# Kernel optimization log

Hardware: AMD Instinct MI355X
Metric: run time of the kernel (lower is better)

## Reference

```python
import jax, jax.numpy as jnp
import numpy as np

NUM_LAYERS = 2
HIDDEN = 512


def setup_inputs() -> dict:
    key = jax.random.key(0)
    ks = jax.random.split(key, 5)
    B, T, D, L, H = 32, 512, 512, NUM_LAYERS, HIDDEN
    s = 1.0 / np.sqrt(H)
    return {
        "x": jax.random.normal(ks[0], (B, T, D), dtype=jnp.float32),
        "h0": jnp.zeros((B, L, H), dtype=jnp.float32),
        "c0": jnp.zeros((B, L, H), dtype=jnp.float32),
        "Wx": jax.random.normal(ks[1], (L, 4 * H, D), dtype=jnp.float32) * s,
        "bx": jax.random.normal(ks[2], (L, 4 * H), dtype=jnp.float32) * s,
        "Wh": jax.random.normal(ks[3], (L, 4 * H, H), dtype=jnp.float32) * s,
        "bh": jax.random.normal(ks[4], (L, 4 * H), dtype=jnp.float32) * s,
    }


def _lstm_forward(x, h0, c0, Wx, bx, Wh, bh):
    # x: [B,T,D]; h0,c0: [B,L,H]; Wx/Wh: [L,4H,*]; gate order (i,f,g,o)
    L, H = Wx.shape[0], Wx.shape[2]

    def step(carry, x_t):
        h, c = carry  # [B,L,H]
        inp = x_t  # [B,D]
        new_h, new_c = [], []
        for l in range(L):
            gates = (inp @ Wx[l].T + bx[l]) + (h[:, l] @ Wh[l].T + bh[l])  # [B,4H]
            i_g, f_g, g_g, o_g = jnp.split(gates, 4, axis=-1)
            c_l = jax.nn.sigmoid(f_g) * c[:, l] + jax.nn.sigmoid(i_g) * jnp.tanh(g_g)
            h_l = jax.nn.sigmoid(o_g) * jnp.tanh(c_l)
            new_h.append(h_l)
            new_c.append(c_l)
            inp = h_l
        return (jnp.stack(new_h, axis=1), jnp.stack(new_c, axis=1)), inp

    (h_n, c_n), ys = jax.lax.scan(step, (h0, c0), jnp.swapaxes(x, 0, 1))
    output = jnp.swapaxes(ys, 0, 1)  # [B,T,H]
    # torch module returns h_n/c_n swapped to [num_layers, batch, hidden]
    return output, (jnp.swapaxes(h_n, 0, 1), jnp.swapaxes(c_n, 0, 1))


def reference(x, h0, c0, Wx, bx, Wh, bh):
    return _lstm_forward(x, h0, c0, Wx, bx, Wh, bh)
```

## Files before the change

### kernel.cpp

```cpp
#include <hip/hip_runtime.h>
#include <hip/hip_bf16.h>

typedef __bf16 bf16x8 __attribute__((ext_vector_type(8)));
typedef float f32x4 __attribute__((ext_vector_type(4)));
typedef unsigned long long u64;

#define MFMA16(a, b, c) __builtin_amdgcn_mfma_f32_16x16x32_bf16((a), (b), (c), 0, 0, 0)

#define HN_OFF 8388608ull
#define CN_OFF 8421376ull

__device__ __forceinline__ float sigf(float x) { return 1.0f / (1.0f + __expf(-x)); }
__device__ __forceinline__ float b2f(unsigned short u) {
    union { unsigned u; float f; } c; c.u = ((unsigned)u) << 16; return c.f;
}
__device__ __forceinline__ unsigned short f2u(float f) {
    __hip_bfloat16 h = __float2bfloat16(f); return *(unsigned short*)&h;
}

__device__ __forceinline__ u64 gload8(const void* p) {
    return __hip_atomic_load((const u64*)p, __ATOMIC_RELAXED, __HIP_MEMORY_SCOPE_AGENT);
}
__device__ __forceinline__ void gstore4(void* p, unsigned v) {
    __hip_atomic_store((unsigned*)p, v, __ATOMIC_RELAXED, __HIP_MEMORY_SCOPE_AGENT);
}

__device__ __forceinline__ void split8(const float* p, bf16x8& hi, bf16x8& lo) {
    union { __hip_bfloat16 h[8]; bf16x8 v; } uh, ul;
    #pragma unroll
    for (int i = 0; i < 8; ++i) {
        __hip_bfloat16 e = __float2bfloat16(p[i]);
        uh.h[i] = e;
        ul.h[i] = __float2bfloat16(p[i] - __bfloat162float(e));
    }
    hi = uh.v; lo = ul.v;
}

__global__ __launch_bounds__(256) void lstm_detect(
    const unsigned* __restrict__ Wq, unsigned* __restrict__ dflag,
    unsigned* __restrict__ flags)
{
    for (int j = threadIdx.x; j < 1024; j += 256) flags[j] = 0;
    if (threadIdx.x < 64) {
        int lane = threadIdx.x;
        int bad = 0;
        #pragma unroll
        for (int i = 0; i < 4; ++i) {
            unsigned u = Wq[(size_t)(lane + i * 64) * 4093];
            float v = b2f((unsigned short)(u & 0xFFFFu));
            if (!(v == v) || fabsf(v) > 100.0f) ++bad;
        }
        #pragma unroll
        for (int off = 32; off; off >>= 1) bad += __shfl_down(bad, off, 64);
        if (lane == 0) *dflag = (bad > 32) ? 1u : 0u;
    }
}

__global__ __launch_bounds__(256) void lstm_init(
    const void* __restrict__ h0v, const void* __restrict__ c0v,
    __hip_bfloat16* __restrict__ h0hi, __hip_bfloat16* __restrict__ h0lo,
    __hip_bfloat16* __restrict__ h1hi, __hip_bfloat16* __restrict__ h1lo,
    float* __restrict__ cws, const unsigned* __restrict__ dflag)
{
    const bool f32 = (*dflag != 0);
    int i = blockIdx.x * 256 + threadIdx.x;
    int b = i >> 9, n = i & 511;
    float f0, f1, g0, g1;
    if (f32) {
        const float* h = (const float*)h0v; const float* c = (const float*)c0v;
        f0 = h[(b * 2 + 0) * 512 + n];  f1 = h[(b * 2 + 1) * 512 + n];
        g0 = c[(b * 2 + 0) * 512 + n];  g1 = c[(b * 2 + 1) * 512 + n];
    } else {
        const unsigned short* h = (const unsigned short*)h0v;
        const unsigned short* c = (const unsigned short*)c0v;
        f0 = b2f(h[(b * 2 + 0) * 512 + n]);  f1 = b2f(h[(b * 2 + 1) * 512 + n]);
        g0 = b2f(c[(b * 2 + 0) * 512 + n]);  g1 = b2f(c[(b * 2 + 1) * 512 + n]);
    }
    __hip_bfloat16 e0 = __float2bfloat16(f0), e1 = __float2bfloat16(f1);
    h0hi[i] = e0; h0lo[i] = __float2bfloat16(f0 - __bfloat162float(e0));
    h1hi[i] = e1; h1lo[i] = __float2bfloat16(f1 - __bfloat162float(e1));
    cws[i] = g0;  cws[16384 + i] = g1;
}

__global__ __launch_bounds__(256, 1) void lstm_seq(
    const void* __restrict__ xv,
    const void* __restrict__ Wxv, const void* __restrict__ bxv,
    const void* __restrict__ Whv, const void* __restrict__ bhv,
    __hip_bfloat16* __restrict__ h0hi, __hip_bfloat16* __restrict__ h0lo,
    __hip_bfloat16* __restrict__ h1hi, __hip_bfloat16* __restrict__ h1lo,
    const float* __restrict__ cws, unsigned* __restrict__ flags,
    const unsigned* __restrict__ dflag, void* __restrict__ outv)
{
    const bool f32 = (*dflag != 0);
    const int p  = blockIdx.x & 1;
    const int wt = blockIdx.x >> 1;
    const int tid = threadIdx.x;
    const int q = tid >> 6, lane = tid & 63;
    const int n16 = lane & 15, quad = lane >> 4;
    const int colg = q * 512 + wt * 16 + n16;

    __shared__ __align__(16) char smem[131072];
    __shared__ float gbuf[2176];

    float* outf = (float*)outv;
    __hip_bfloat16* outh = (__hip_bfloat16*)outv;

    bf16x8 wa[16], wal[16], wr[16], wrl[16];
    if (f32) {
        const float* WA = (const float*)Wxv + ((size_t)(p * 2048 + colg)) * 512;
        const float* WR = (const float*)Whv + ((size_t)(p * 2048 + colg)) * 512;
        #pragma unroll
        for (int kk = 0; kk < 16; ++kk) {
            split8(WA + kk * 32 + quad * 8, wa[kk], wal[kk]);
            split8(WR + kk * 32 + quad * 8, wr[kk], wrl[kk]);
        }
    } else {
        const unsigned short* WA = (const unsigned short*)Wxv + ((size_t)(p * 2048 + colg)) * 512;
        const unsigned short* WR = (const unsigned short*)Whv + ((size_t)(p * 2048 + colg)) * 512;
        union { uint4 u; bf16x8 v; } cvu;
        #pragma unroll
        for (int kk = 0; kk < 16; ++kk) {
            cvu.u = *(const uint4*)(WA + kk * 32 + quad * 8); wa[kk] = cvu.v;
            cvu.u = *(const uint4*)(WR + kk * 32 + quad * 8); wr[kk] = cvu.v;
        }
    }
    float bias;
    if (f32) bias = ((const float*)bxv)[p * 2048 + colg] + ((const float*)bhv)[p * 2048 + colg];
    else     bias = b2f(((const unsigned short*)bxv)[p * 2048 + colg])
                  + b2f(((const unsigned short*)bhv)[p * 2048 + colg]);

    const int e0 = tid * 2;
    const int pbb = e0 >> 4;
    const int pn0 = e0 & 15;
    float cv[2];
    cv[0] = cws[p * 16384 + pbb * 512 + wt * 16 + pn0];
    cv[1] = cws[p * 16384 + pbb * 512 + wt * 16 + pn0 + 1];

    const unsigned short* xb = (const unsigned short*)xv;

    #define STAGE_X_BF16(T)                                                      \
        { _Pragma("unroll")                                                      \
          for (int j = 0; j < 8; ++j) {                                          \
              int L = j * 256 + tid;                                             \
              int rem = L & 127;                                                 \
              int row = ((rem >> 6) << 4) + (rem & 15);                          \
              int kcol = ((L >> 7) << 5) + (((rem >> 4) & 3) << 3);              \
              *(uint4*)(smem + (L << 4)) =                                       \
                  *(const uint4*)(xb + ((size_t)row * 512 + (T)) * 512 + kcol);  \
          } }

    if (p == 0 && !f32) STAGE_X_BF16(0);

    for (int k = 0; k <= 512; ++k) {
        const bool doComp = (p == 0) ? (k < 512) : (k > 0);

        if (doComp) {
            const int t = (p == 0) ? k : (k - 1);
            const __hip_bfloat16* Ahi = h0hi + (k & 1) * 16384;
            const __hip_bfloat16* Alo = h0lo + (k & 1) * 16384;
            const __hip_bfloat16* Rhi = (p == 0) ? h0hi + (k & 1) * 16384
                                                 : h1hi + ((k + 1) & 1) * 16384;
            const __hip_bfloat16* Rlo = (p == 0) ? h0lo + (k & 1) * 16384
                                                 : h1lo + ((k + 1) & 1) * 16384;

            if (p == 1) {
                #pragma unroll
                for (int hp = 0; hp < 2; ++hp) {
                    u64 vA[8], vB[8], vR[8], vL[8];
                    #pragma unroll
                    for (int jj = 0; jj < 4; ++jj) {
                        int L = (hp * 4 + jj) * 256 + tid;
                        int rem = L & 127;
                        int row = ((rem >> 6) << 4) + (rem & 15);
                        int kcol = ((L >> 7) << 5) + (((rem >> 4) & 3) << 3);
                        size_t hoff = (size_t)row * 512 + kcol;
                        vA[jj*2] = gload8(Ahi + hoff); vA[jj*2+1] = gload8(Ahi + hoff + 4);
                        vB[jj*2] = gload8(Alo + hoff); vB[jj*2+1] = gload8(Alo + hoff + 4);
                        vR[jj*2] = gload8(Rhi + hoff); vR[jj*2+1] = gload8(Rhi + hoff + 4);
                        vL[jj*2] = gload8(Rlo + hoff); vL[jj*2+1] = gload8(Rlo + hoff + 4);
                    }
                    #pragma unroll
                    for (int jj = 0; jj < 4; ++jj) {
                        int L = (hp * 4 + jj) * 256 + tid;
                        u64* dA = (u64*)(smem + (L << 4));
                        u64* dB = (u64*)(smem + 32768 + (L << 4));
                        u64* dR = (u64*)(smem + 65536 + (L << 4));
                        u64* dL = (u64*)(smem + 98304 + (L << 4));
                        dA[0] = vA[jj*2]; dA[1] = vA[jj*2+1];
                        dB[0] = vB[jj*2]; dB[1] = vB[jj*2+1];
                        dR[0] = vR[jj*2]; dR[1] = vR[jj*2+1];
                        dL[0] = vL[jj*2]; dL[1] = vL[jj*2+1];
                    }
                }
            } else {
                u64 vR[16], vL[16];
                #pragma unroll
                for (int j = 0; j < 8; ++j) {
                    int L = j * 256 + tid;
                    int rem = L & 127;
                    int row = ((rem >> 6) << 4) + (rem & 15);
                    int kcol = ((L >> 7) << 5) + (((rem >> 4) & 3) << 3);
                    size_t hoff = (size_t)row * 512 + kcol;
                    vR[j*2] = gload8(Rhi + hoff); vR[j*2+1] = gload8(Rhi + hoff + 4);
                    vL[j*2] = gload8(Rlo + hoff); vL[j*2+1] = gload8(Rlo + hoff + 4);
                }
                #pragma unroll
                for (int j = 0; j < 8; ++j) {
                    int L = j * 256 + tid;
                    u64* dR = (u64*)(smem + 65536 + (L << 4));
                    u64* dL = (u64*)(smem + 98304 + (L << 4));
                    dR[0] = vR[j*2]; dR[1] = vR[j*2+1];
                    dL[0] = vL[j*2]; dL[1] = vL[j*2+1];
                }
                if (f32) {
                    #pragma unroll
                    for (int j = 0; j < 8; ++j) {
                        int L = j * 256 + tid;
                        int rem = L & 127;
                        int row = ((rem >> 6) << 4) + (rem & 15);
                        int kcol = ((L >> 7) << 5) + (((rem >> 4) & 3) << 3);
                        const float* xp = (const float*)xv + ((size_t)row * 512 + t) * 512 + kcol;
                        bf16x8 hi, lo;
                        split8(xp, hi, lo);
                        *(bf16x8*)(smem + (L << 4)) = hi;
                        *(bf16x8*)(smem + 32768 + (L << 4)) = lo;
                    }
                }
            }
            __syncthreads();

            const char* sl = smem + (lane << 4);
            f32x4 acc0 = {bias, bias, bias, bias};
            f32x4 acc1 = {bias, bias, bias, bias};
            if (f32) {
                #pragma unroll
                for (int kk = 0; kk < 16; ++kk) {
                    bf16x8 Aha = *(const bf16x8*)(sl + kk * 2048);
                    bf16x8 Ahb = *(const bf16x8*)(sl + kk * 2048 + 1024);
                    bf16x8 Ala = *(const bf16x8*)(sl + 32768 + kk * 2048);
                    bf16x8 Alb = *(const bf16x8*)(sl + 32768 + kk * 2048 + 1024);
                    bf16x8 Rha = *(const bf16x8*)(sl + 65536 + kk * 2048);
                    bf16x8 Rhb = *(const bf16x8*)(sl + 65536 + kk * 2048 + 1024);
                    bf16x8 Rla = *(const bf16x8*)(sl + 98304 + kk * 2048);
                    bf16x8 Rlb = *(const bf16x8*)(sl + 98304 + kk * 2048 + 1024);
                    acc0 = MFMA16(Aha, wa[kk], acc0);
                    acc0 = MFMA16(Aha, wal[kk], acc0);
                    acc0 = MFMA16(Ala, wa[kk], acc0);
                    acc0 = MFMA16(Rha, wr[kk], acc0);
                    acc0 = MFMA16(Rha, wrl[kk], acc0);
                    acc0 = MFMA16(Rla, wr[kk], acc0);
                    acc1 = MFMA16(Ahb, wa[kk], acc1);
                    acc1 = MFMA16(Ahb, wal[kk], acc1);
                    acc1 = MFMA16(Alb, wa[kk], acc1);
                    acc1 = MFMA16(Rhb, wr[kk], acc1);
                    acc1 = MFMA16(Rhb, wrl[kk], acc1);
                    acc1 = MFMA16(Rlb, wr[kk], acc1);
                }
            } else if (p == 1) {
                #pragma unroll
                for (int kk = 0; kk < 16; ++kk) {
                    bf16x8 Aha = *(const bf16x8*)(sl + kk * 2048);
                    bf16x8 Ahb = *(const bf16x8*)(sl + kk * 2048 + 1024);
                    bf16x8 Ala = *(const bf16x8*)(sl + 32768 + kk * 2048);
                    bf16x8 Alb = *(const bf16x8*)(sl + 32768 + kk * 2048 + 1024);
                    bf16x8 Rha = *(const bf16x8*)(sl + 65536 + kk * 2048);
                    bf16x8 Rhb = *(const bf16x8*)(sl + 65536 + kk * 2048 + 1024);
                    bf16x8 Rla = *(const bf16x8*)(sl + 98304 + kk * 2048);
                    bf16x8 Rlb = *(const bf16x8*)(sl + 98304 + kk * 2048 + 1024);
                    acc0 = MFMA16(Aha, wa[kk], acc0);
                    acc0 = MFMA16(Ala, wa[kk], acc0);
                    acc0 = MFMA16(Rha, wr[kk], acc0);
                    acc0 = MFMA16(Rla, wr[kk], acc0);
                    acc1 = MFMA16(Ahb, wa[kk], acc1);
                    acc1 = MFMA16(Alb, wa[kk], acc1);
                    acc1 = MFMA16(Rhb, wr[kk], acc1);
                    acc1 = MFMA16(Rlb, wr[kk], acc1);
                }
            } else {
                #pragma unroll
                for (int kk = 0; kk < 16; ++kk) {
                    bf16x8 Aha = *(const bf16x8*)(sl + kk * 2048);
                    bf16x8 Ahb = *(const bf16x8*)(sl + kk * 2048 + 1024);
                    bf16x8 Rha = *(const bf16x8*)(sl + 65536 + kk * 2048);
                    bf16x8 Rhb = *(const bf16x8*)(sl + 65536 + kk * 2048 + 1024);
                    bf16x8 Rla = *(const bf16x8*)(sl + 98304 + kk * 2048);
                    bf16x8 Rlb = *(const bf16x8*)(sl + 98304 + kk * 2048 + 1024);
                    acc0 = MFMA16(Aha, wa[kk], acc0);
                    acc0 = MFMA16(Rha, wr[kk], acc0);
                    acc0 = MFMA16(Rla, wr[kk], acc0);
                    acc1 = MFMA16(Ahb, wa[kk], acc1);
                    acc1 = MFMA16(Rhb, wr[kk], acc1);
                    acc1 = MFMA16(Rlb, wr[kk], acc1);
                }
            }
            __syncthreads();

            #pragma unroll
            for (int r = 0; r < 4; ++r) {
                gbuf[(q * 32 + quad * 4 + r) * 17 + n16]      = acc0[r];
                gbuf[(q * 32 + 16 + quad * 4 + r) * 17 + n16] = acc1[r];
            }
            __syncthreads();

            __hip_bfloat16* Ohi = (p == 0) ? h0hi + ((k + 1) & 1) * 16384
                                           : h1hi + (k & 1) * 16384;
            __hip_bfloat16* Olo = (p == 0) ? h0lo + ((k + 1) & 1) * 16384
                                           : h1lo + (k & 1) * 16384;
            float rh[2], rc[2];
            #pragma unroll
            for (int j = 0; j < 2; ++j) {
                int n = pn0 + j;
                float ig = gbuf[(0 * 32 + pbb) * 17 + n];
                float fg = gbuf[(1 * 32 + pbb) * 17 + n];
                float gg = gbuf[(2 * 32 + pbb) * 17 + n];
                float og = gbuf[(3 * 32 + pbb) * 17 + n];
                float cnew = sigf(fg) * cv[j] + sigf(ig) * tanhf(gg);
                cv[j] = cnew;
                rc[j] = cnew;
                rh[j] = sigf(og) * tanhf(cnew);
            }
            unsigned phi = 0, plo = 0, pcn = 0;
            #pragma unroll
            for (int j = 0; j < 2; ++j) {
                unsigned short hu = f2u(rh[j]);
                unsigned short lu = f2u(rh[j] - b2f(hu));
                phi |= ((unsigned)hu) << (16 * j);
                plo |= ((unsigned)lu) << (16 * j);
                pcn |= ((unsigned)f2u(rc[j])) << (16 * j);
            }
            const int idx = pbb * 512 + wt * 16 + pn0;
            gstore4(Ohi + idx, phi);
            gstore4(Olo + idx, plo);

            __syncthreads();
            if (k < 512 && tid == 0)
                __hip_atomic_store(&flags[blockIdx.x * 16], (unsigned)(k + 1),
                                   __ATOMIC_RELAXED, __HIP_MEMORY_SCOPE_AGENT);

            if (p == 1) {
                size_t oidx = ((size_t)pbb * 512 + t) * 512 + wt * 16 + pn0;
                if (f32) { outf[oidx] = rh[0]; outf[oidx + 1] = rh[1]; }
                else     { *(unsigned*)(outh + oidx) = phi; }
                if (k == 512) {
                    if (f32) {
                        outf[HN_OFF + 16384 + idx] = rh[0]; outf[HN_OFF + 16385 + idx] = rh[1];
                        outf[CN_OFF + 16384 + idx] = rc[0]; outf[CN_OFF + 16385 + idx] = rc[1];
                    } else {
                        *(unsigned*)(outh + HN_OFF + 16384 + idx) = phi;
                        *(unsigned*)(outh + CN_OFF + 16384 + idx) = pcn;
                    }
                }
            } else if (k == 511) {
                if (f32) {
                    outf[HN_OFF + idx] = rh[0]; outf[HN_OFF + idx + 1] = rh[1];
                    outf[CN_OFF + idx] = rc[0]; outf[CN_OFF + idx + 1] = rc[1];
                } else {
                    *(unsigned*)(outh + HN_OFF + idx) = phi;
                    *(unsigned*)(outh + CN_OFF + idx) = pcn;
                }
            }
            if (p == 0 && !f32 && k + 1 < 512) STAGE_X_BF16(k + 1);
        } else {
            if (k < 512 && tid == 0)
                __hip_atomic_store(&flags[blockIdx.x * 16], (unsigned)(k + 1),
                                   __ATOMIC_RELAXED, __HIP_MEMORY_SCOPE_AGENT);
        }

        if (k < 512) {
            if (tid < 64) {
                while (__hip_atomic_load(&flags[tid * 16],
                                         __ATOMIC_RELAXED, __HIP_MEMORY_SCOPE_AGENT)
                       < (unsigned)(k + 1))
                    __builtin_amdgcn_s_sleep(1);
            }
            __syncthreads();
        }
    }
}

extern "C" void kernel_launch(void* const* d_in, const int* in_sizes, int n_in,
                              void* d_out, int out_size, void* d_ws, size_t ws_size,
                              hipStream_t stream)
{
    const void* x  = d_in[0];
    const void* h0 = d_in[1];
    const void* c0 = d_in[2];
    const void* Wx = d_in[3];
    const void* bx = d_in[4];
    const void* Wh = d_in[5];
    const void* bh = d_in[6];

    char* ws = (char*)d_ws;
    __hip_bfloat16* h0hi = (__hip_bfloat16*)(ws);
    __hip_bfloat16* h0lo = (__hip_bfloat16*)(ws + 65536);
    __hip_bfloat16* h1hi = (__hip_bfloat16*)(ws + 131072);
    __hip_bfloat16* h1lo = (__hip_bfloat16*)(ws + 196608);
    float*          cws  = (float*)(ws + 262144);
    unsigned*       flags = (unsigned*)(ws + 393216);
    unsigned*       dflag = (unsigned*)(ws + 397312);

    lstm_detect<<<1, 256, 0, stream>>>((const unsigned*)Wx, dflag, flags);
    lstm_init<<<64, 256, 0, stream>>>(h0, c0, h0hi, h0lo, h1hi, h1lo, cws, dflag);
    lstm_seq<<<64, 256, 0, stream>>>(x, Wx, bx, Wh, bh,
                                     h0hi, h0lo, h1hi, h1lo, cws, flags, dflag, d_out);
}
```

Before: 6.950 ms.

## Replace global per-step barrier with split-phase flag polling and 4-deep h0 ring

Replaces the all-blocks barrier at the end of each timestep with targeted polling of the even (layer-0) or odd (layer-1) block flags right before each operand is needed. Layer-0 blocks now compute the input projection before waiting for the recurrent state, and the layer-0 hidden buffer becomes a 4-deep ring so layer 0 can run ahead of layer 1 by more than one step. This is meant to hide barrier latency and let the two layers pipeline more loosely, at the cost of more workspace, an extra sync after staging, and more complex correctness reasoning around ring reuse. The f32 x staging is also moved to layer-0 prefetch after the step.

```diff
diff --git a/kernel.cpp b/kernel.cpp
--- a/kernel.cpp
+++ b/kernel.cpp
@@ -149,229 +149,222 @@
                   *(const uint4*)(xb + ((size_t)row * 512 + (T)) * 512 + kcol);  \
           } }
 
-    if (p == 0 && !f32) STAGE_X_BF16(0);
+    #define STAGE_X_F32(T)                                                       \
+        { _Pragma("unroll")                                                      \
+          for (int j = 0; j < 8; ++j) {                                          \
+              int L = j * 256 + tid;                                             \
+              int rem = L & 127;                                                 \
+              int row = ((rem >> 6) << 4) + (rem & 15);                          \
+              int kcol = ((L >> 7) << 5) + (((rem >> 4) & 3) << 3);              \
+              const float* xp = (const float*)xv + ((size_t)row * 512 + (T)) * 512 + kcol; \
+              bf16x8 hi_, lo_;                                                   \
+              split8(xp, hi_, lo_);                                              \
+              *(bf16x8*)(smem + (L << 4)) = hi_;                                 \
+              *(bf16x8*)(smem + 32768 + (L << 4)) = lo_;                         \
+          } }
+
+    #define GATHER2(SH, SL, DH, DL)                                              \
+        { u64 vH[16], vL[16];                                                    \
+          _Pragma("unroll")                                                      \
+          for (int j = 0; j < 8; ++j) {                                          \
+              int L = j * 256 + tid;                                             \
+              int rem = L & 127;                                                 \
+              int row = ((rem >> 6) << 4) + (rem & 15);                          \
+              int kcol = ((L >> 7) << 5) + (((rem >> 4) & 3) << 3);              \
+              size_t hoff = (size_t)row * 512 + kcol;                            \
+              vH[j*2] = gload8((SH) + hoff); vH[j*2+1] = gload8((SH) + hoff + 4);\
+              vL[j*2] = gload8((SL) + hoff); vL[j*2+1] = gload8((SL) + hoff + 4);\
+          }                                                                      \
+          _Pragma("unroll")                                                      \
+          for (int j = 0; j < 8; ++j) {                                          \
+              int L = j * 256 + tid;                                             \
+              u64* dH = (u64*)(smem + (DH) + (L << 4));                          \
+              u64* dL = (u64*)(smem + (DL) + (L << 4));                          \
+              dH[0] = vH[j*2]; dH[1] = vH[j*2+1];                                \
+              dL[0] = vL[j*2]; dL[1] = vL[j*2+1];                                \
+          } }
+
+    #define POLL(THR_E, THR_O)                                                   \
+        { if (tid < 64) {                                                        \
+              int thr_ = ((tid & 1) == 0) ? (THR_E) : (THR_O);                   \
+              if (thr_ > 0) {                                                    \
+                  while ((int)__hip_atomic_load(&flags[tid * 16],                \
+                             __ATOMIC_RELAXED, __HIP_MEMORY_SCOPE_AGENT) < thr_) \
+                      __builtin_amdgcn_s_sleep(1);                               \
+              }                                                                  \
+          }                                                                      \
+          __syncthreads(); }
+
+    #define MM_A_F32()                                                           \
+        { _Pragma("unroll")                                                      \
+          for (int kk = 0; kk < 16; ++kk) {                                      \
+              bf16x8 Aha = *(const bf16x8*)(sl + kk * 2048);                     \
+              bf16x8 Ahb = *(const bf16x8*)(sl + kk * 2048 + 1024);              \
+              bf16x8 Ala = *(const bf16x8*)(sl + 32768 + kk * 2048);             \
+              bf16x8 Alb = *(const bf16x8*)(sl + 32768 + kk * 2048 + 1024);      \
+              acc0 = MFMA16(Aha, wa[kk], acc0);  acc1 = MFMA16(Ahb, wa[kk], acc1);   \
+              acc0 = MFMA16(Aha, wal[kk], acc0); acc1 = MFMA16(Ahb, wal[kk], acc1);  \
+              acc0 = MFMA16(Ala, wa[kk], acc0);  acc1 = MFMA16(Alb, wa[kk], acc1);   \
+          } }
+
+    #define MM_R_F32()                                                           \
+        { _Pragma("unroll")                                                      \
+          for (int kk = 0; kk < 16; ++kk) {                                      \
+              bf16x8 Rha = *(const bf16x8*)(sl + 65536 + kk * 2048);             \
+              bf16x8 Rhb = *(const bf16x8*)(sl + 65536 + kk * 2048 + 1024);      \
+              bf16x8 Rla = *(const bf16x8*)(sl + 98304 + kk * 2048);             \
+              bf16x8 Rlb = *(const bf16x8*)(sl + 98304 + kk * 2048 + 1024);      \
+              acc0 = MFMA16(Rha, wr[kk], acc0);  acc1 = MFMA16(Rhb, wr[kk], acc1);   \
+              acc0 = MFMA16(Rha, wrl[kk], acc0); acc1 = MFMA16(Rhb, wrl[kk], acc1);  \
+              acc0 = MFMA16(Rla, wr[kk], acc0);  acc1 = MFMA16(Rlb, wr[kk], acc1);   \
+          } }
+
+    #define MM_A_BF16_P0()                                                       \
+        { _Pragma("unroll")                                                      \
+          for (int kk = 0; kk < 16; ++kk) {                                      \
+              bf16x8 Aha = *(const bf16x8*)(sl + kk * 2048);                     \
+              bf16x8 Ahb = *(const bf16x8*)(sl + kk * 2048 + 1024);              \
+              acc0 = MFMA16(Aha, wa[kk], acc0);  acc1 = MFMA16(Ahb, wa[kk], acc1);   \
+          } }
+
+    #define MM_A_BF16_P1()                                                       \
+        { _Pragma("unroll")                                                      \
+          for (int kk = 0; kk < 16; ++kk) {                                      \
+              bf16x8 Aha = *(const bf16x8*)(sl + kk * 2048);                     \
+              bf16x8 Ahb = *(const bf16x8*)(sl + kk * 2048 + 1024);              \
+              bf16x8 Ala = *(const bf16x8*)(sl + 32768 + kk * 2048);             \
+              bf16x8 Alb = *(const bf16x8*)(sl + 32768 + kk * 2048 + 1024);      \
+              acc0 = MFMA16(Aha, wa[kk], acc0);  acc1 = MFMA16(Ahb, wa[kk], acc1);   \
+              acc0 = MFMA16(Ala, wa[kk], acc0);  acc1 = MFMA16(Alb, wa[kk], acc1);   \
+          } }
+
+    #define MM_R_BF16()                                                          \
+        { _Pragma("unroll")                                                      \
+          for (int kk = 0; kk < 16; ++kk) {                                      \
+              bf16x8 Rha = *(const bf16x8*)(sl + 65536 + kk * 2048);             \
+              bf16x8 Rhb = *(const bf16x8*)(sl + 65536 + kk * 2048 + 1024);      \
+              bf16x8 Rla = *(const bf16x8*)(sl + 98304 + kk * 2048);             \
+              bf16x8 Rlb = *(const bf16x8*)(sl + 98304 + kk * 2048 + 1024);      \
+              acc0 = MFMA16(Rha, wr[kk], acc0);  acc1 = MFMA16(Rhb, wr[kk], acc1);   \
+              acc0 = MFMA16(Rla, wr[kk], acc0);  acc1 = MFMA16(Rlb, wr[kk], acc1);   \
+          } }
+
+    if (p == 0) {
+        if (f32) { STAGE_X_F32(0) } else { STAGE_X_BF16(0) }
+        __syncthreads();
+    }
 
     for (int k = 0; k <= 512; ++k) {
         const bool doComp = (p == 0) ? (k < 512) : (k > 0);
-
-        if (doComp) {
-            const int t = (p == 0) ? k : (k - 1);
-            const __hip_bfloat16* Ahi = h0hi + (k & 1) * 16384;
-            const __hip_bfloat16* Alo = h0lo + (k & 1) * 16384;
-            const __hip_bfloat16* Rhi = (p == 0) ? h0hi + (k & 1) * 16384
-                                                 : h1hi + ((k + 1) & 1) * 16384;
-            const __hip_bfloat16* Rlo = (p == 0) ? h0lo + (k & 1) * 16384
-                                                 : h1lo + ((k + 1) & 1) * 16384;
-
-            if (p == 1) {
-                #pragma unroll
-                for (int hp = 0; hp < 2; ++hp) {
-                    u64 vA[8], vB[8], vR[8], vL[8];
-                    #pragma unroll
-                    for (int jj = 0; jj < 4; ++jj) {
-                        int L = (hp * 4 + jj) * 256 + tid;
-                        int rem = L & 127;
-                        int row = ((rem >> 6) << 4) + (rem & 15);
-                        int kcol = ((L >> 7) << 5) + (((rem >> 4) & 3) << 3);
-                        size_t hoff = (size_t)row * 512 + kcol;
-                        vA[jj*2] = gload8(Ahi + hoff); vA[jj*2+1] = gload8(Ahi + hoff + 4);
-                        vB[jj*2] = gload8(Alo + hoff); vB[jj*2+1] = gload8(Alo + hoff + 4);
-                        vR[jj*2] = gload8(Rhi + hoff); vR[jj*2+1] = gload8(Rhi + hoff + 4);
-                        vL[jj*2] = gload8(Rlo + hoff); vL[jj*2+1] = gload8(Rlo + hoff + 4);
-                    }
-                    #pragma unroll
-                    for (int jj = 0; jj < 4; ++jj) {
-                        int L = (hp * 4 + jj) * 256 + tid;
-                        u64* dA = (u64*)(smem + (L << 4));
-                        u64* dB = (u64*)(smem + 32768 + (L << 4));
-                        u64* dR = (u64*)(smem + 65536 + (L << 4));
-                        u64* dL = (u64*)(smem + 98304 + (L << 4));
-                        dA[0] = vA[jj*2]; dA[1] = vA[jj*2+1];
-                        dB[0] = vB[jj*2]; dB[1] = vB[jj*2+1];
-                        dR[0] = vR[jj*2]; dR[1] = vR[jj*2+1];
-                        dL[0] = vL[jj*2]; dL[1] = vL[jj*2+1];
-                    }
-                }
-            } else {
-                u64 vR[16], vL[16];
-                #pragma unroll
-                for (int j = 0; j < 8; ++j) {
-                    int L = j * 256 + tid;
-                    int rem = L & 127;
-                    int row = ((rem >> 6) << 4) + (rem & 15);
-                    int kcol = ((L >> 7) << 5) + (((rem >> 4) & 3) << 3);
-                    size_t hoff = (size_t)row * 512 + kcol;
-                    vR[j*2] = gload8(Rhi + hoff); vR[j*2+1] = gload8(Rhi + hoff + 4);
-                    vL[j*2] = gload8(Rlo + hoff); vL[j*2+1] = gload8(Rlo + hoff + 4);
-                }
-                #pragma unroll
-                for (int j = 0; j < 8; ++j) {
-                    int L = j * 256 + tid;
-                    u64* dR = (u64*)(smem + 65536 + (L << 4));
-                    u64* dL = (u64*)(smem + 98304 + (L << 4));
-                    dR[0] = vR[j*2]; dR[1] = vR[j*2+1];
-                    dL[0] = vL[j*2]; dL[1] = vL[j*2+1];
-                }
-                if (f32) {
-                    #pragma unroll
-                    for (int j = 0; j < 8; ++j) {
-                        int L = j * 256 + tid;
-                        int rem = L & 127;
-                        int row = ((rem >> 6) << 4) + (rem & 15);
-                        int kcol = ((L >> 7) << 5) + (((rem >> 4) & 3) << 3);
-                        const float* xp = (const float*)xv + ((size_t)row * 512 + t) * 512 + kcol;
-                        bf16x8 hi, lo;
-                        split8(xp, hi, lo);
-                        *(bf16x8*)(smem + (L << 4)) = hi;
-                        *(bf16x8*)(smem + 32768 + (L << 4)) = lo;
-                    }
-                }
-            }
-            __syncthreads();
-
-            const char* sl = smem + (lane << 4);
-            f32x4 acc0 = {bias, bias, bias, bias};
-            f32x4 acc1 = {bias, bias, bias, bias};
-            if (f32) {
-                #pragma unroll
-                for (int kk = 0; kk < 16; ++kk) {
-                    bf16x8 Aha = *(const bf16x8*)(sl + kk * 2048);
-                    bf16x8 Ahb = *(const bf16x8*)(sl + kk * 2048 + 1024);
-                    bf16x8 Ala = *(const bf16x8*)(sl + 32768 + kk * 2048);
-                    bf16x8 Alb = *(const bf16x8*)(sl + 32768 + kk * 2048 + 1024);
-                    bf16x8 Rha = *(const bf16x8*)(sl + 65536 + kk * 2048);
-                    bf16x8 Rhb = *(const bf16x8*)(sl + 65536 + kk * 2048 + 1024);
-                    bf16x8 Rla = *(const bf16x8*)(sl + 98304 + kk * 2048);
-                    bf16x8 Rlb = *(const bf16x8*)(sl + 98304 + kk * 2048 + 1024);
-                    acc0 = MFMA16(Aha, wa[kk], acc0);
-                    acc0 = MFMA16(Aha, wal[kk], acc0);
-                    acc0 = MFMA16(Ala, wa[kk], acc0);
-                    acc0 = MFMA16(Rha, wr[kk], acc0);
-                    acc0 = MFMA16(Rha, wrl[kk], acc0);
-                    acc0 = MFMA16(Rla, wr[kk], acc0);
-                    acc1 = MFMA16(Ahb, wa[kk], acc1);
-                    acc1 = MFMA16(Ahb, wal[kk], acc1);
-                    acc1 = MFMA16(Alb, wa[kk], acc1);
-                    acc1 = MFMA16(Rhb, wr[kk], acc1);
-                    acc1 = MFMA16(Rhb, wrl[kk], acc1);
-                    acc1 = MFMA16(Rlb, wr[kk], acc1);
-                }
-            } else if (p == 1) {
-                #pragma unroll
-                for (int kk = 0; kk < 16; ++kk) {
-                    bf16x8 Aha = *(const bf16x8*)(sl + kk * 2048);
-                    bf16x8 Ahb = *(const bf16x8*)(sl + kk * 2048 + 1024);
-                    bf16x8 Ala = *(const bf16x8*)(sl + 32768 + kk * 2048);
-                    bf16x8 Alb = *(const bf16x8*)(sl + 32768 + kk * 2048 + 1024);
-                    bf16x8 Rha = *(const bf16x8*)(sl + 65536 + kk * 2048);
-                    bf16x8 Rhb = *(const bf16x8*)(sl + 65536 + kk * 2048 + 1024);
-                    bf16x8 Rla = *(const bf16x8*)(sl + 98304 + kk * 2048);
-                    bf16x8 Rlb = *(const bf16x8*)(sl + 98304 + kk * 2048 + 1024);
-                    acc0 = MFMA16(Aha, wa[kk], acc0);
-                    acc0 = MFMA16(Ala, wa[kk], acc0);
-                    acc0 = MFMA16(Rha, wr[kk], acc0);
-                    acc0 = MFMA16(Rla, wr[kk], acc0);
-                    acc1 = MFMA16(Ahb, wa[kk], acc1);
-                    acc1 = MFMA16(Alb, wa[kk], acc1);
-                    acc1 = MFMA16(Rhb, wr[kk], acc1);
-                    acc1 = MFMA16(Rlb, wr[kk], acc1);
-                }
-            } else {
-                #pragma unroll
-                for (int kk = 0; kk < 16; ++kk) {
-                    bf16x8 Aha = *(const bf16x8*)(sl + kk * 2048);
-                    bf16x8 Ahb = *(const bf16x8*)(sl + kk * 2048 + 1024);
-                    bf16x8 Rha = *(const bf16x8*)(sl + 65536 + kk * 2048);
-                    bf16x8 Rhb = *(const bf16x8*)(sl + 65536 + kk * 2048 + 1024);
-                    bf16x8 Rla = *(const bf16x8*)(sl + 98304 + kk * 2048);
-                    bf16x8 Rlb = *(const bf16x8*)(sl + 98304 + kk * 2048 + 1024);
-                    acc0 = MFMA16(Aha, wa[kk], acc0);
-                    acc0 = MFMA16(Rha, wr[kk], acc0);
-                    acc0 = MFMA16(Rla, wr[kk], acc0);
-                    acc1 = MFMA16(Ahb, wa[kk], acc1);
-                    acc1 = MFMA16(Rhb, wr[kk], acc1);
-                    acc1 = MFMA16(Rlb, wr[kk], acc1);
-                }
-            }
-            __syncthreads();
-
-            #pragma unroll
-            for (int r = 0; r < 4; ++r) {
-                gbuf[(q * 32 + quad * 4 + r) * 17 + n16]      = acc0[r];
-                gbuf[(q * 32 + 16 + quad * 4 + r) * 17 + n16] = acc1[r];
-            }
-            __syncthreads();
-
-            __hip_bfloat16* Ohi = (p == 0) ? h0hi + ((k + 1) & 1) * 16384
-                                           : h1hi + (k & 1) * 16384;
-            __hip_bfloat16* Olo = (p == 0) ? h0lo + ((k + 1) & 1) * 16384
-                                           : h1lo + (k & 1) * 16384;
-            float rh[2], rc[2];
-            #pragma unroll
-            for (int j = 0; j < 2; ++j) {
-                int n = pn0 + j;
-                float ig = gbuf[(0 * 32 + pbb) * 17 + n];
-                float fg = gbuf[(1 * 32 + pbb) * 17 + n];
-                float gg = gbuf[(2 * 32 + pbb) * 17 + n];
-                float og = gbuf[(3 * 32 + pbb) * 17 + n];
-                float cnew = sigf(fg) * cv[j] + sigf(ig) * tanhf(gg);
-                cv[j] = cnew;
-                rc[j] = cnew;
-                rh[j] = sigf(og) * tanhf(cnew);
-            }
-            unsigned phi = 0, plo = 0, pcn = 0;
-            #pragma unroll
-            for (int j = 0; j < 2; ++j) {
-                unsigned short hu = f2u(rh[j]);
-                unsigned short lu = f2u(rh[j] - b2f(hu));
-                phi |= ((unsigned)hu) << (16 * j);
-                plo |= ((unsigned)lu) << (16 * j);
-                pcn |= ((unsigned)f2u(rc[j])) << (16 * j);
-            }
-            const int idx = pbb * 512 + wt * 16 + pn0;
-            gstore4(Ohi + idx, phi);
-            gstore4(Olo + idx, plo);
-
-            __syncthreads();
-            if (k < 512 && tid == 0)
+        if (!doComp) {
+            if (tid == 0)
                 __hip_atomic_store(&flags[blockIdx.x * 16], (unsigned)(k + 1),
                                    __ATOMIC_RELAXED, __HIP_MEMORY_SCOPE_AGENT);
-
-            if (p == 1) {
-                size_t oidx = ((size_t)pbb * 512 + t) * 512 + wt * 16 + pn0;
-                if (f32) { outf[oidx] = rh[0]; outf[oidx + 1] = rh[1]; }
-                else     { *(unsigned*)(outh + oidx) = phi; }
-                if (k == 512) {
-                    if (f32) {
-                        outf[HN_OFF + 16384 + idx] = rh[0]; outf[HN_OFF + 16385 + idx] = rh[1];
-                        outf[CN_OFF + 16384 + idx] = rc[0]; outf[CN_OFF + 16385 + idx] = rc[1];
-                    } else {
-                        *(unsigned*)(outh + HN_OFF + 16384 + idx) = phi;
-                        *(unsigned*)(outh + CN_OFF + 16384 + idx) = pcn;
-                    }
+            continue;
+        }
+
+        const char* sl = smem + (lane << 4);
+        f32x4 acc0 = {bias, bias, bias, bias};
+        f32x4 acc1 = {bias, bias, bias, bias};
+        const int t = (p == 0) ? k : (k - 1);
+
+        if (p == 0) {
+            if (f32) { MM_A_F32() } else { MM_A_BF16_P0() }
+            POLL(k, k - 2)
+            {
+                const __hip_bfloat16* Rhi = h0hi + (size_t)(k & 3) * 16384;
+                const __hip_bfloat16* Rlo = h0lo + (size_t)(k & 3) * 16384;
+                GATHER2(Rhi, Rlo, 65536, 98304)
+            }
+            __syncthreads();
+            if (f32) { MM_R_F32() } else { MM_R_BF16() }
+        } else {
+            POLL(k, 0)
+            {
+                const __hip_bfloat16* Ahi = h0hi + (size_t)(k & 3) * 16384;
+                const __hip_bfloat16* Alo = h0lo + (size_t)(k & 3) * 16384;
+                GATHER2(Ahi, Alo, 0, 32768)
+            }
+            __syncthreads();
+            if (f32) { MM_A_F32() } else { MM_A_BF16_P1() }
+            POLL(0, k)
+            {
+                const __hip_bfloat16* Rhi = h1hi + (size_t)((k + 1) & 1) * 16384;
+                const __hip_bfloat16* Rlo = h1lo + (size_t)((k + 1) & 1) * 16384;
+                GATHER2(Rhi, Rlo, 65536, 98304)
+            }
+            __syncthreads();
+            if (f32) { MM_R_F32() } else { MM_R_BF16() }
+        }
+
+        #pragma unroll
+        for (int r = 0; r < 4; ++r) {
+            gbuf[(q * 32 + quad * 4 + r) * 17 + n16]      = acc0[r];
+            gbuf[(q * 32 + 16 + quad * 4 + r) * 17 + n16] = acc1[r];
+        }
+        __syncthreads();
+
+        __hip_bfloat16* Ohi = (p == 0) ? h0hi + (size_t)((k + 1) & 3) * 16384
+                                       : h1hi + (size_t)(k & 1) * 16384;
+        __hip_bfloat16* Olo = (p == 0) ? h0lo + (size_t)((k + 1) & 3) * 16384
+                                       : h1lo + (size_t)(k & 1) * 16384;
+        float rh[2], rc[2];
+        #pragma unroll
+        for (int j = 0; j < 2; ++j) {
+            int n = pn0 + j;
+            float ig = gbuf[(0 * 32 + pbb) * 17 + n];
+            float fg = gbuf[(1 * 32 + pbb) * 17 + n];
+            float gg = gbuf[(2 * 32 + pbb) * 17 + n];
+            float og = gbuf[(3 * 32 + pbb) * 17 + n];
+            float cnew = sigf(fg) * cv[j] + sigf(ig) * tanhf(gg);
+            cv[j] = cnew;
+            rc[j] = cnew;
+            rh[j] = sigf(og) * tanhf(cnew);
+        }
+        unsigned phi = 0, plo = 0, pcn = 0;
+        #pragma unroll
+        for (int j = 0; j < 2; ++j) {
+            unsigned short hu = f2u(rh[j]);
+            unsigned short lu = f2u(rh[j] - b2f(hu));
+            phi |= ((unsigned)hu) << (16 * j);
+            plo |= ((unsigned)lu) << (16 * j);
+            pcn |= ((unsigned)f2u(rc[j])) << (16 * j);
+        }
+        const int idx = pbb * 512 + wt * 16 + pn0;
+        gstore4(Ohi + idx, phi);
+        gstore4(Olo + idx, plo);
+
+        __syncthreads();
+        if (tid == 0)
+            __hip_atomic_store(&flags[blockIdx.x * 16], (unsigned)(k + 1),
+                               __ATOMIC_RELAXED, __HIP_MEMORY_SCOPE_AGENT);
+
+        if (p == 1) {
+            size_t oidx = ((size_t)pbb * 512 + t) * 512 + wt * 16 + pn0;
+            if (f32) { outf[oidx] = rh[0]; outf[oidx + 1] = rh[1]; }
+            else     { *(unsigned*)(outh + oidx) = phi; }
+            if (k == 512) {
+                if (f32) {
+                    outf[HN_OFF + 16384 + idx] = rh[0]; outf[HN_OFF + 16385 + idx] = rh[1];
+                    outf[CN_OFF + 16384 + idx] = rc[0]; outf[CN_OFF + 16385 + idx] = rc[1];
+                } else {
+                    *(unsigned*)(outh + HN_OFF + 16384 + idx) = phi;
+                    *(unsigned*)(outh + CN_OFF + 16384 + idx) = pcn;
                 }
-            } else if (k == 511) {
-                if (f32) {
-                    outf[HN_OFF + idx] = rh[0]; outf[HN_OFF + idx + 1] = rh[1];
-                    outf[CN_OFF + idx] = rc[0]; outf[CN_OFF + idx + 1] = rc[1];
-                } else {
-                    *(unsigned*)(outh + HN_OFF + idx) = phi;
-                    *(unsigned*)(outh + CN_OFF + idx) = pcn;
-                }
-            }
-            if (p == 0 && !f32 && k + 1 < 512) STAGE_X_BF16(k + 1);
-        } else {
-            if (k < 512 && tid == 0)
-                __hip_atomic_store(&flags[blockIdx.x * 16], (unsigned)(k + 1),
-                                   __ATOMIC_RELAXED, __HIP_MEMORY_SCOPE_AGENT);
-        }
-
-        if (k < 512) {
-            if (tid < 64) {
-                while (__hip_atomic_load(&flags[tid * 16],
-                                         __ATOMIC_RELAXED, __HIP_MEMORY_SCOPE_AGENT)
-                       < (unsigned)(k + 1))
-                    __builtin_amdgcn_s_sleep(1);
+            }
+        } else if (k == 511) {
+            if (f32) {
+                outf[HN_OFF + idx] = rh[0]; outf[HN_OFF + idx + 1] = rh[1];
+                outf[CN_OFF + idx] = rc[0]; outf[CN_OFF + idx + 1] = rc[1];
+            } else {
+                *(unsigned*)(outh + HN_OFF + idx) = phi;
+                *(unsigned*)(outh + CN_OFF + idx) = pcn;
+            }
+        }
+
+        if (p == 0) {
+            if (k + 1 < 512) {
+                if (f32) { STAGE_X_F32(k + 1) } else { STAGE_X_BF16(k + 1) }
             }
             __syncthreads();
         }
@@ -392,12 +385,12 @@
 
     char* ws = (char*)d_ws;
     __hip_bfloat16* h0hi = (__hip_bfloat16*)(ws);
-    __hip_bfloat16* h0lo = (__hip_bfloat16*)(ws + 65536);
-    __hip_bfloat16* h1hi = (__hip_bfloat16*)(ws + 131072);
-    __hip_bfloat16* h1lo = (__hip_bfloat16*)(ws + 196608);
-    float*          cws  = (float*)(ws + 262144);
-    unsigned*       flags = (unsigned*)(ws + 393216);
-    unsigned*       dflag = (unsigned*)(ws + 397312);
+    __hip_bfloat16* h0lo = (__hip_bfloat16*)(ws + 131072);
+    __hip_bfloat16* h1hi = (__hip_bfloat16*)(ws + 262144);
+    __hip_bfloat16* h1lo = (__hip_bfloat16*)(ws + 327680);
+    float*          cws  = (float*)(ws + 393216);
+    unsigned*       flags = (unsigned*)(ws + 524288);
+    unsigned*       dflag = (unsigned*)(ws + 528384);
 
     lstm_detect<<<1, 256, 0, stream>>>((const unsigned*)Wx, dflag, flags);
     lstm_init<<<64, 256, 0, stream>>>(h0, c0, h0hi, h0lo, h1hi, h1lo, cws, dflag);
```

Result: faster. 6.215 ms (-10.6%).
